# Kernel tuning notes

Measured on AMD Instinct MI355X. Metric: run time of the kernel, lower is better.

Reference implementation:

```python
import jax, jax.numpy as jnp
import numpy as np
from jax import lax

B, C, H, W = 4, 512, 48, 48
R = 8            # inter_rate -> spatial q/k channels = C // R
C4 = C // 4      # chl_attention query channels
N = H * W


def _conv1x1(x, w, b=None):
    # x: (B,C,H,W), w: (O,C)
    y = jnp.einsum('bchw,oc->bohw', x, w)
    if b is not None:
        y = y + b[None, :, None, None]
    return y


def _conv3x3(x, w):
    # w: (O,I,3,3), SAME padding, no bias
    return lax.conv_general_dilated(x, w, (1, 1), 'SAME',
                                    dimension_numbers=('NCHW', 'OIHW', 'NCHW'))


def _bn_relu(x, scale, bias):
    # eval-mode BatchNorm folded into per-channel scale/bias, then ReLU
    return jax.nn.relu(x * scale[None, :, None, None] + bias[None, :, None, None])


def _masked_softmax(e, mask):
    # softmax restricted to mask>0 positions (== exp(e)*mask / sum(exp(e)*mask))
    neg = jnp.finfo(e.dtype).min
    z = jnp.where(mask[None] > 0, e, neg)
    return jax.nn.softmax(z, axis=-1)


def _chl(x, qw, qs, qb, ew, eb):
    # channel attention block (chl_attention)
    b, c, h, w = x.shape
    n = h * w
    q = jnp.einsum('bchw,oc->bohw', x, qw)                 # (B,C4,H,W)
    q = jax.nn.relu(q * qs[None, :, None, None] + qb[None, :, None, None])
    q = q.reshape(b, C4, n)
    k = x.reshape(b, c, n)
    energy = jnp.einsum('bqn,bcn->bqc', q, k)              # (B,C4,C)
    expand = jnp.einsum('oq,bqc->boc', ew, energy) + eb[None, :, None]  # (B,C,C)
    en = jnp.max(expand, -1, keepdims=True) - expand
    attn = jax.nn.softmax(en, -1)                          # (B,C,C)
    out = jnp.einsum('bcd,bdn->bcn', attn, k)
    return out.reshape(b, c, h, w)


def setup_inputs() -> dict:
    key = jax.random.key(0)
    ks = jax.random.split(key, 32)
    f = jnp.float32
    s = lambda k, shp, sc: (sc * jax.random.normal(k, shp)).astype(f)
    inp = {}
    inp['x'] = s(ks[0], (B, C, H, W), 1.0)
    Cr = C // R
    inp['wq'] = s(ks[1], (Cr, C), 1.0 / np.sqrt(C))
    inp['bq'] = s(ks[2], (Cr,), 0.02)
    inp['wk'] = s(ks[3], (Cr, C), 1.0 / np.sqrt(C))
    inp['bk'] = s(ks[4], (Cr,), 0.02)
    inp['wv0'] = s(ks[5], (C, C), 1.0 / np.sqrt(C))
    inp['bv0'] = s(ks[6], (C,), 0.02)
    inp['conv1_w'] = s(ks[7], (C, C, 3, 3), 1.0 / np.sqrt(9 * C))
    inp['conv1_s'] = (1.0 + 0.1 * jax.random.normal(ks[8], (C,))).astype(f)
    inp['conv1_b'] = s(ks[9], (C,), 0.05)
    inp['conv2_w'] = s(ks[10], (C, C, 3, 3), 1.0 / np.sqrt(9 * C))
    inp['conv2_s'] = (1.0 + 0.1 * jax.random.normal(ks[11], (C,))).astype(f)
    inp['conv2_b'] = s(ks[12], (C,), 0.05)
    inp['gamma'] = jnp.full((1,), 0.5, f)
    inp['gamma1'] = jnp.full((1,), 0.5, f)
    inp['gamma2'] = jnp.full((1,), 0.5, f)
    # chl_attention #1 params
    inp['c1_qw'] = s(ks[13], (C4, C), 1.0 / np.sqrt(C))
    inp['c1_qs'] = (1.0 + 0.1 * jax.random.normal(ks[14], (C4,))).astype(f)
    inp['c1_qb'] = s(ks[15], (C4,), 0.05)
    inp['c1_ew'] = s(ks[16], (C, C4), 1.0 / np.sqrt(C4))
    inp['c1_eb'] = s(ks[17], (C,), 0.02)
    # chl_attention #2 params
    inp['c2_qw'] = s(ks[18], (C4, C), 1.0 / np.sqrt(C))
    inp['c2_qs'] = (1.0 + 0.1 * jax.random.normal(ks[19], (C4,))).astype(f)
    inp['c2_qb'] = s(ks[20], (C4,), 0.05)
    inp['c2_ew'] = s(ks[21], (C, C4), 1.0 / np.sqrt(C4))
    inp['c2_eb'] = s(ks[22], (C,), 0.02)
    # binary (N,N) masks: random sparsity + diagonal so every row has support
    eye = jnp.eye(N, dtype=f)
    m1 = (jax.random.uniform(ks[23], (N, N)) < 0.25).astype(f)
    m2 = (jax.random.uniform(ks[24], (N, N)) < 0.10).astype(f)
    inp['mask1'] = jnp.maximum(m1, eye)
    inp['mask2'] = jnp.maximum(m2, eye)
    return inp


def reference(x, wq, bq, wk, bk, wv0, bv0, conv1_w, conv1_s, conv1_b,
              conv2_w, conv2_s, conv2_b, gamma, gamma1, gamma2,
              c1_qw, c1_qs, c1_qb, c1_ew, c1_eb,
              c2_qw, c2_qs, c2_qb, c2_ew, c2_eb, mask1, mask2):
    b, c, h, w = x.shape
    n = h * w
    q = _conv1x1(x, wq, bq).reshape(b, -1, n)   # (B,Cr,N)
    k = _conv1x1(x, wk, bk).reshape(b, -1, n)   # (B,Cr,N)
    energy = jnp.einsum('bqn,bqm->bnm', q, k)   # (B,N,N)
    attn0 = jax.nn.softmax(energy, -1)
    attn1 = _masked_softmax(energy, mask1)
    attn2 = _masked_softmax(energy, mask2)
    v = _conv1x1(x, wv0, bv0).reshape(b, c, n)
    # pass 0 (unmasked)
    out0 = jnp.einsum('bcn,bmn->bcm', v, attn0).reshape(b, c, h, w)
    out0 = gamma[0] * out0 + x
    out0 = _bn_relu(_conv3x3(out0, conv1_w), conv1_s, conv1_b)
    # pass 1 (mask1, channel-attn value)
    v1 = _chl(out0, c1_qw, c1_qs, c1_qb, c1_ew, c1_eb).reshape(b, c, n)
    out1 = jnp.einsum('bcn,bmn->bcm', v1, attn1).reshape(b, c, h, w)
    out1 = gamma1[0] * out1 + out0
    out1 = _bn_relu(_conv3x3(out1, conv2_w), conv2_s, conv2_b)
    # pass 2 (mask2)
    v2 = _chl(out1, c2_qw, c2_qs, c2_qb, c2_ew, c2_eb).reshape(b, c, n)
    out2 = jnp.einsum('bcn,bmn->bcm', v2, attn2).reshape(b, c, h, w)
    out = gamma2[0] * out2 + out1
    return out
```

## Files before the change

### kernel.cpp

```cpp
#include <hip/hip_runtime.h>

#define B_  4
#define C_  512
#define H_  48
#define W_  48
#define N_  2304
#define CR_ 64
#define C4_ 128
#define TK  16
#define LDSP 68
#define PW  50
#define PN  2500
#define KW  4608

typedef short  s16x8 __attribute__((ext_vector_type(8)));
typedef float  f32x4 __attribute__((ext_vector_type(4)));

__device__ __forceinline__ unsigned short f2bf(float f) {
  union { float f; unsigned int u; } v; v.f = f;
  const unsigned int u = v.u;
  return (unsigned short)((u + 0x7FFFu + ((u >> 16) & 1u)) >> 16);
}
__device__ __forceinline__ float bf2f(unsigned short h) {
  union { unsigned int u; float f; } v; v.u = ((unsigned int)h) << 16;
// ... 28 lines not shown
  for (int kk = 0; kk < TK; ++kk) {
    const float4 a4 = *(const float4*)(&As[kk][ty * 4]);
    const float4 b4 = *(const float4*)(&Bs[kk][tx * 4]);
    const float av[4] = {a4.x, a4.y, a4.z, a4.w};
    const float bv[4] = {b4.x, b4.y, b4.z, b4.w};
#pragma unroll
    for (int i = 0; i < 4; ++i)
#pragma unroll
      for (int j = 0; j < 4; ++j)
        acc[i][j] = fmaf(av[i], bv[j], acc[i][j]);
  }
}

__global__ __launch_bounds__(256)
void gemm_nn(const float* __restrict__ A, long long aStrideB, int lda,
             const float* __restrict__ B, long long bStrideB, int ldb,
             float* __restrict__ Y, long long yStrideB, int ldy,
             int K,
             const float* __restrict__ scale, const float* __restrict__ bias, int relu)
{
  __shared__ float As[TK][LDSP], Bs[TK][LDSP];
  const int b  = blockIdx.z;
  const int m0 = blockIdx.y * 64, n0 = blockIdx.x * 64;
  const int tid = threadIdx.x, tx = tid & 15, ty = tid >> 4;
  const int ia = tid >> 2, ka = (tid & 3) * 4;
  const int jb = tid & 63, kb = (tid >> 6) * 4;
  const float* Ab = A + (size_t)b * aStrideB;
  const float* Bb = B + (size_t)b * bStrideB;
  float acc[4][4] = {};
  for (int k0 = 0; k0 < K; k0 += TK) {
    const float4 a4 = *(const float4*)(Ab + (size_t)(m0 + ia) * lda + k0 + ka);
    As[ka + 0][ia] = a4.x; As[ka + 1][ia] = a4.y;
    As[ka + 2][ia] = a4.z; As[ka + 3][ia] = a4.w;
#pragma unroll
    for (int t = 0; t < 4; ++t)
      Bs[kb + t][jb] = Bb[(size_t)(k0 + kb + t) * ldb + n0 + jb];
    __syncthreads();
    mm16(As, Bs, acc, ty, tx);
    __syncthreads();
  }
  float* Yb = Y + (size_t)b * yStrideB;
#pragma unroll
  for (int i = 0; i < 4; ++i) {
    const int row = m0 + ty * 4 + i;
    const float s = scale ? scale[row] : 1.f;
    const float bb = bias ? bias[row] : 0.f;
    float4 o;
    o.x = acc[i][0] * s + bb; o.y = acc[i][1] * s + bb;
    o.z = acc[i][2] * s + bb; o.w = acc[i][3] * s + bb;
    if (relu) {
      o.x = fmaxf(o.x, 0.f); o.y = fmaxf(o.y, 0.f);
      o.z = fmaxf(o.z, 0.f); o.w = fmaxf(o.w, 0.f);
    }
    *(float4*)(Yb + (size_t)row * ldy + n0 + tx * 4) = o;
  }
}

__global__ __launch_bounds__(256)
void gemm_nt(const float* __restrict__ A, long long aStrideB, int lda,
             const float* __restrict__ B, long long bStrideB, int ldb,
             float* __restrict__ Y, long long yStrideB, int ldy, int K)
{
  __shared__ float As[TK][LDSP], Bs[TK][LDSP];
  const int b  = blockIdx.z;
  const int m0 = blockIdx.y * 64, n0 = blockIdx.x * 64;
  const int tid = threadIdx.x, tx = tid & 15, ty = tid >> 4;
  const int ia = tid >> 2, ka = (tid & 3) * 4;
  const float* Ab = A + (size_t)b * aStrideB;
  const float* Bb = B + (size_t)b * bStrideB;
  float acc[4][4] = {};
  for (int k0 = 0; k0 < K; k0 += TK) {
    const float4 a4 = *(const float4*)(Ab + (size_t)(m0 + ia) * lda + k0 + ka);
    As[ka + 0][ia] = a4.x; As[ka + 1][ia] = a4.y;
    As[ka + 2][ia] = a4.z; As[ka + 3][ia] = a4.w;
    const float4 b4 = *(const float4*)(Bb + (size_t)(n0 + ia) * ldb + k0 + ka);
    Bs[ka + 0][ia] = b4.x; Bs[ka + 1][ia] = b4.y;
    Bs[ka + 2][ia] = b4.z; Bs[ka + 3][ia] = b4.w;
    __syncthreads();
    mm16(As, Bs, acc, ty, tx);
    __syncthreads();
  }
  float* Yb = Y + (size_t)b * yStrideB;
#pragma unroll
  for (int i = 0; i < 4; ++i) {
    const int row = m0 + ty * 4 + i;
    float4 o = {acc[i][0], acc[i][1], acc[i][2], acc[i][3]};
    *(float4*)(Yb + (size_t)row * ldy + n0 + tx * 4) = o;
  }
}

__global__ __launch_bounds__(256)
void gemm_nt_splitk(const float* __restrict__ A, long long aStrideB, int lda,
                    const float* __restrict__ B, long long bStrideB, int ldb,
                    float* __restrict__ Y, long long yStrideB, int ldy, int K)
{
  __shared__ float As[TK][LDSP], Bs[TK][LDSP];
  const int z = blockIdx.z, b = z >> 2, ks = z & 3;
  const int kBeg = ks * (K / 4), kEnd = kBeg + K / 4;
  const int m0 = blockIdx.y * 64, n0 = blockIdx.x * 64;
  const int tid = threadIdx.x, tx = tid & 15, ty = tid >> 4;
  const int ia = tid >> 2, ka = (tid & 3) * 4;
  const float* Ab = A + (size_t)b * aStrideB;
  const float* Bb = B + (size_t)b * bStrideB;
  float acc[4][4] = {};
  for (int k0 = kBeg; k0 < kEnd; k0 += TK) {
    const float4 a4 = *(const float4*)(Ab + (size_t)(m0 + ia) * lda + k0 + ka);
    As[ka + 0][ia] = a4.x; As[ka + 1][ia] = a4.y;
    As[ka + 2][ia] = a4.z; As[ka + 3][ia] = a4.w;
    const float4 b4 = *(const float4*)(Bb + (size_t)(n0 + ia) * ldb + k0 + ka);
    Bs[ka + 0][ia] = b4.x; Bs[ka + 1][ia] = b4.y;
    Bs[ka + 2][ia] = b4.z; Bs[ka + 3][ia] = b4.w;
    __syncthreads();
    mm16(As, Bs, acc, ty, tx);
    __syncthreads();
  }
  float* Yb = Y + (size_t)b * yStrideB;
#pragma unroll
  for (int i = 0; i < 4; ++i) {
    const int row = m0 + ty * 4 + i;
#pragma unroll
    for (int j = 0; j < 4; ++j)
      atomicAdd(Yb + (size_t)row * ldy + n0 + tx * 4 + j, acc[i][j]);
  }
}

__global__ __launch_bounds__(256)
void zero_buf(float4* __restrict__ p, int n4)
{
  const int i = blockIdx.x * 256 + threadIdx.x;
  if (i < n4) p[i] = float4{0.f, 0.f, 0.f, 0.f};
}

__global__ __launch_bounds__(256)
void gemm_tn(const float* __restrict__ A, long long aStrideB, int lda,
             const float* __restrict__ B, long long bStrideB, int ldb,
             float* __restrict__ Y, long long yStrideB, int ldy, int K)
{
  __shared__ float As[TK][LDSP], Bs[TK][LDSP];
  const int b  = blockIdx.z;
// ... 85 lines not shown
      const float4 x2 = *(const float4*)(src + 8);
      const float4 x3 = *(const float4*)(src + 12);
      s16x8 p0 = { (short)f2bf(x0.x), (short)f2bf(x0.y), (short)f2bf(x0.z), (short)f2bf(x0.w),
                   (short)f2bf(x1.x), (short)f2bf(x1.y), (short)f2bf(x1.z), (short)f2bf(x1.w) };
      s16x8 p1 = { (short)f2bf(x2.x), (short)f2bf(x2.y), (short)f2bf(x2.z), (short)f2bf(x2.w),
                   (short)f2bf(x3.x), (short)f2bf(x3.y), (short)f2bf(x3.z), (short)f2bf(x3.w) };
      *(s16x8*)&Bs[sRow][sK]     = p0;
      *(s16x8*)&Bs[sRow][sK + 8] = p1;
    }
    __syncthreads();
#pragma unroll
    for (int kc = 0; kc < 2; ++kc) {
      const s16x8 a0 = *(const s16x8*)&As[wm * 32 + lrow     ][kc * 32 + lk8];
      const s16x8 a1 = *(const s16x8*)&As[wm * 32 + 16 + lrow][kc * 32 + lk8];
      const s16x8 b0 = *(const s16x8*)&Bs[wn * 32 + lrow     ][kc * 32 + lk8];
      const s16x8 b1 = *(const s16x8*)&Bs[wn * 32 + 16 + lrow][kc * 32 + lk8];
      acc[0][0] = __builtin_amdgcn_mfma_f32_16x16x32_bf16(a0, b0, acc[0][0], 0, 0, 0);
      acc[0][1] = __builtin_amdgcn_mfma_f32_16x16x32_bf16(a0, b1, acc[0][1], 0, 0, 0);
      acc[1][0] = __builtin_amdgcn_mfma_f32_16x16x32_bf16(a1, b0, acc[1][0], 0, 0, 0);
      acc[1][1] = __builtin_amdgcn_mfma_f32_16x16x32_bf16(a1, b1, acc[1][1], 0, 0, 0);
    }
    __syncthreads();
  }

  const float g = gammaPtr ? gammaPtr[0] : 0.f;
  const float* Rb = Resid ? Resid + (size_t)b * rSB : nullptr;
#pragma unroll
  for (int mt = 0; mt < 2; ++mt)
#pragma unroll
    for (int nt = 0; nt < 2; ++nt) {
      const int col = n0 + wn * 32 + nt * 16 + lrow;
      const int rbase = m0 + wm * 32 + mt * 16 + (lane >> 4) * 4;
#pragma unroll
      for (int i = 0; i < 4; ++i) {
        const int row = rbase + i;
        float v = acc[mt][nt][i];
        if (Rb) {
          v = g * v + Rb[(size_t)row * ldy + col];
        } else {
          const float s  = scale ? scale[row] : 1.f;
          const float bb = bias ? bias[row] : 0.f;
          v = v * s + bb;
          if (relu) v = fmaxf(v, 0.f);
        }
        if (outBf16)
          ((unsigned short*)Yv)[(size_t)b * ySB + (size_t)row * ldy + col] = f2bf(v);
        else
          ((float*)Yv)[(size_t)b * ySB + (size_t)row * ldy + col] = v;
      }
    }
}

__global__ __launch_bounds__(256)
void pad_split(const float* __restrict__ X, unsigned short* __restrict__ Xh,
               unsigned short* __restrict__ Xl)
{
  __shared__ float t[64][65];
  const int b = blockIdx.x, n0 = blockIdx.y * 64;
  const int tid = threadIdx.x;
  const float* Xb = X + (size_t)b * C_ * N_;
  unsigned short* Xhb = Xh + (size_t)b * PN * C_;
  unsigned short* Xlb = Xl + (size_t)b * PN * C_;
  for (int cs = 0; cs < 8; ++cs) {
    const int c0 = cs * 64;
    __syncthreads();
#pragma unroll
    for (int i = 0; i < 16; ++i) {
      const int cc = i * 4 + (tid >> 6);
      t[cc][tid & 63] = Xb[(size_t)(c0 + cc) * N_ + n0 + (tid & 63)];
    }
    __syncthreads();
    const int cc = tid & 63;
#pragma unroll
    for (int i = 0; i < 16; ++i) {
      const int nn = i * 4 + (tid >> 6);
      const int n = n0 + nn;
      const float v = t[cc][nn];
      const unsigned short hh = f2bf(v);
      const unsigned short ll = f2bf(v - bf2f(hh));
      const size_t p = (size_t)((n / 48 + 1) * PW + (n % 48) + 1) * C_ + c0 + cc;
      Xhb[p] = hh; Xlb[p] = ll;
    }
  }
}

__global__ __launch_bounds__(256)
void zero_ring(unsigned short* __restrict__ Xh, unsigned short* __restrict__ Xl)
{
  const int b = blockIdx.y, r = blockIdx.x;
  int pcol;
  if (r < 50)       pcol = r;
  else if (r < 100) pcol = 49 * PW + (r - 50);
  else if (r < 148) pcol = (r - 100 + 1) * PW;
  else              pcol = (r - 148 + 1) * PW + 49;
  unsigned int* h = (unsigned int*)(Xh + ((size_t)b * PN + pcol) * C_);
  unsigned int* l = (unsigned int*)(Xl + ((size_t)b * PN + pcol) * C_);
  h[threadIdx.x] = 0u;
  l[threadIdx.x] = 0u;
}

__global__ __launch_bounds__(256)
void wsplit(const float* __restrict__ W, unsigned short* __restrict__ Wh,
            unsigned short* __restrict__ Wl)
{
  const int o = blockIdx.x, tap = blockIdx.y;
#pragma unroll
  for (int i = 0; i < 2; ++i) {
    const int c = threadIdx.x + i * 256;
    const float v = W[(size_t)o * KW + c * 9 + tap];
    const unsigned short hh = f2bf(v);
    Wh[(size_t)o * KW + tap * C_ + c] = hh;
    Wl[(size_t)o * KW + tap * C_ + c] = f2bf(v - bf2f(hh));
  }
}

__global__ __launch_bounds__(256)
void tr_bf16(const float* __restrict__ X, unsigned short* __restrict__ T)
{
  __shared__ float t[64][65];
  const int b = blockIdx.x, n0 = blockIdx.y * 64;
  const int tid = threadIdx.x;
  const float* Xb = X + (size_t)b * C_ * N_;
  unsigned short* Tb = T + (size_t)b * N_ * C_;
  for (int cs = 0; cs < 8; ++cs) {
    const int c0 = cs * 64;
    __syncthreads();
#pragma unroll
    for (int i = 0; i < 16; ++i) {
      const int cc = i * 4 + (tid >> 6);
      t[cc][tid & 63] = Xb[(size_t)(c0 + cc) * N_ + n0 + (tid & 63)];
    }
    __syncthreads();
    const int cc = tid & 63;
#pragma unroll
    for (int i = 0; i < 16; ++i) {
      const int nn = i * 4 + (tid >> 6);
      Tb[(size_t)(n0 + nn) * C_ + c0 + cc] = f2bf(t[cc][nn]);
    }
  }
}

__global__ __launch_bounds__(256)
void mfma_conv2(const unsigned short* __restrict__ Xh, const unsigned short* __restrict__ Xl,
                const unsigned short* __restrict__ Wh, const unsigned short* __restrict__ Wl,
                const float* __restrict__ sc, const float* __restrict__ bi,
                float* __restrict__ Y)
{
  __shared__ unsigned short Ah[64][72], Al[64][72];
  __shared__ unsigned short Bh[64][72], Bl[64][72];
  const int b  = blockIdx.z;
  const int m0 = blockIdx.y * 64, n0 = blockIdx.x * 64;
  const int tid  = threadIdx.x;
  const int lane = tid & 63, wave = tid >> 6;
  const int wm = wave >> 1, wn = wave & 1;
  const int lrow = lane & 15, lk8 = (lane >> 4) * 8;
  const int sRow = tid >> 2, sK = (tid & 3) * 16;
  const int nj = n0 + sRow;
  const int pbase = (nj / 48 + 1) * PW + (nj % 48) + 1;
  const unsigned short* Xhb = Xh + (size_t)b * PN * C_;
  const unsigned short* Xlb = Xl + (size_t)b * PN * C_;
  f32x4 acc[2][2] = {};

#pragma unroll
  for (int tap = 0; tap < 9; ++tap) {
    const int toff = (tap / 3 - 1) * PW + (tap % 3 - 1);
    const size_t bofs = (size_t)(pbase + toff) * C_;
    const size_t wrow = (size_t)(m0 + sRow) * KW + (size_t)tap * C_;
    for (int cs = 0; cs < 8; ++cs) {
      const int c0 = cs * 64;
      {
        const unsigned short* s = Wh + wrow + c0 + sK;
        *(s16x8*)&Ah[sRow][sK]     = *(const s16x8*)(s);
        *(s16x8*)&Ah[sRow][sK + 8] = *(const s16x8*)(s + 8);
        const unsigned short* s2 = Wl + wrow + c0 + sK;
        *(s16x8*)&Al[sRow][sK]     = *(const s16x8*)(s2);
        *(s16x8*)&Al[sRow][sK + 8] = *(const s16x8*)(s2 + 8);
      }
      {
        const unsigned short* s = Xhb + bofs + c0 + sK;
        *(s16x8*)&Bh[sRow][sK]     = *(const s16x8*)(s);
        *(s16x8*)&Bh[sRow][sK + 8] = *(const s16x8*)(s + 8);
        const unsigned short* s2 = Xlb + bofs + c0 + sK;
        *(s16x8*)&Bl[sRow][sK]     = *(const s16x8*)(s2);
        *(s16x8*)&Bl[sRow][sK + 8] = *(const s16x8*)(s2 + 8);
      }
      __syncthreads();
#pragma unroll
      for (int kc = 0; kc < 2; ++kc) {
        const s16x8 ah0 = *(const s16x8*)&Ah[wm * 32 + lrow     ][kc * 32 + lk8];
        const s16x8 ah1 = *(const s16x8*)&Ah[wm * 32 + 16 + lrow][kc * 32 + lk8];
        const s16x8 al0 = *(const s16x8*)&Al[wm * 32 + lrow     ][kc * 32 + lk8];
        const s16x8 al1 = *(const s16x8*)&Al[wm * 32 + 16 + lrow][kc * 32 + lk8];
        const s16x8 bh0 = *(const s16x8*)&Bh[wn * 32 + lrow     ][kc * 32 + lk8];
        const s16x8 bh1 = *(const s16x8*)&Bh[wn * 32 + 16 + lrow][kc * 32 + lk8];
        const s16x8 bl0 = *(const s16x8*)&Bl[wn * 32 + lrow     ][kc * 32 + lk8];
        const s16x8 bl1 = *(const s16x8*)&Bl[wn * 32 + 16 + lrow][kc * 32 + lk8];
        acc[0][0] = __builtin_amdgcn_mfma_f32_16x16x32_bf16(ah0, bh0, acc[0][0], 0, 0, 0);
        acc[0][1] = __builtin_amdgcn_mfma_f32_16x16x32_bf16(ah0, bh1, acc[0][1], 0, 0, 0);
        acc[1][0] = __builtin_amdgcn_mfma_f32_16x16x32_bf16(ah1, bh0, acc[1][0], 0, 0, 0);
        acc[1][1] = __builtin_amdgcn_mfma_f32_16x16x32_bf16(ah1, bh1, acc[1][1], 0, 0, 0);
        acc[0][0] = __builtin_amdgcn_mfma_f32_16x16x32_bf16(ah0, bl0, acc[0][0], 0, 0, 0);
        acc[0][1] = __builtin_amdgcn_mfma_f32_16x16x32_bf16(ah0, bl1, acc[0][1], 0, 0, 0);
        acc[1][0] = __builtin_amdgcn_mfma_f32_16x16x32_bf16(ah1, bl0, acc[1][0], 0, 0, 0);
        acc[1][1] = __builtin_amdgcn_mfma_f32_16x16x32_bf16(ah1, bl1, acc[1][1], 0, 0, 0);
        acc[0][0] = __builtin_amdgcn_mfma_f32_16x16x32_bf16(al0, bh0, acc[0][0], 0, 0, 0);
        acc[0][1] = __builtin_amdgcn_mfma_f32_16x16x32_bf16(al0, bh1, acc[0][1], 0, 0, 0);
        acc[1][0] = __builtin_amdgcn_mfma_f32_16x16x32_bf16(al1, bh0, acc[1][0], 0, 0, 0);
        acc[1][1] = __builtin_amdgcn_mfma_f32_16x16x32_bf16(al1, bh1, acc[1][1], 0, 0, 0);
      }
      __syncthreads();
    }
  }

  float* Yb = Y + (size_t)b * C_ * N_;
#pragma unroll
  for (int mt = 0; mt < 2; ++mt)
#pragma unroll
    for (int nt = 0; nt < 2; ++nt) {
      const int col = n0 + wn * 32 + nt * 16 + lrow;
      const int rbase = m0 + wm * 32 + mt * 16 + (lane >> 4) * 4;
#pragma unroll
      for (int i = 0; i < 4; ++i) {
        const int row = rbase + i;
        const float v = fmaxf(acc[mt][nt][i] * sc[row] + bi[row], 0.f);
        Yb[(size_t)row * N_ + col] = v;
      }
    }
}

__global__ __launch_bounds__(256)
void mfma_conv_split(const float* __restrict__ X, const float* __restrict__ Wt,
                     const float* __restrict__ sc, const float* __restrict__ bi,
                     float* __restrict__ Y)
{
  __shared__ unsigned short Ah[64][72], Al[64][72];
  __shared__ unsigned short Bh[64][72], Bl[64][72];
  const int b  = blockIdx.z;
  const int m0 = blockIdx.y * 64, n0 = blockIdx.x * 64;
  const int tid  = threadIdx.x;
  const int lane = tid & 63, wave = tid >> 6;
  const int wm = wave >> 1, wn = wave & 1;
  const int lrow = lane & 15, lk8 = (lane >> 4) * 8;
  const int sRow = tid >> 2, sK = (tid & 3) * 16;
  const int tj = tid & 63, tkg = (tid >> 6) * 16;
  const int n = n0 + tj, yy = n / W_, xx = n - yy * W_;
  const float* Xb = X + (size_t)b * C_ * N_;
  const int K = KW;
  f32x4 acc[2][2] = {};

  for (int k0 = 0; k0 < K; k0 += 64) {
    {
      const float* src = Wt + (size_t)(m0 + sRow) * K + k0 + sK;
      unsigned short h[16], l[16];
#pragma unroll
      for (int t = 0; t < 16; ++t) {
        const float v = src[t];
        const unsigned short hh = f2bf(v);
        h[t] = hh;
        l[t] = f2bf(v - bf2f(hh));
      }
      *(s16x8*)&Ah[sRow][sK]     = *(s16x8*)&h[0];
      *(s16x8*)&Ah[sRow][sK + 8] = *(s16x8*)&h[8];
      *(s16x8*)&Al[sRow][sK]     = *(s16x8*)&l[0];
      *(s16x8*)&Al[sRow][sK + 8] = *(s16x8*)&l[8];
    }
    {
#pragma unroll
      for (int ii = 0; ii < 16; ii += 2) {
        unsigned int ph = 0, pl = 0;
#pragma unroll
        for (int hft = 0; hft < 2; ++hft) {
          const int kg = k0 + tkg + ii + hft;
          const int c = kg / 9, tap = kg - c * 9;
          const int t3 = tap / 3;
          const int iy = yy + t3 - 1, ix = xx + (tap - t3 * 3) - 1;
          float v = 0.f;
          if (iy >= 0 && iy < H_ && ix >= 0 && ix < W_)
            v = Xb[(size_t)c * N_ + iy * W_ + ix];
          const unsigned short hh = f2bf(v);
          const unsigned short ll = f2bf(v - bf2f(hh));
          ph |= ((unsigned int)hh) << (16 * hft);
          pl |= ((unsigned int)ll) << (16 * hft);
        }
        *(unsigned int*)&Bh[tj][tkg + ii] = ph;
        *(unsigned int*)&Bl[tj][tkg + ii] = pl;
      }
    }
    __syncthreads();
#pragma unroll
    for (int kc = 0; kc < 2; ++kc) {
      const s16x8 ah0 = *(const s16x8*)&Ah[wm * 32 + lrow     ][kc * 32 + lk8];
      const s16x8 ah1 = *(const s16x8*)&Ah[wm * 32 + 16 + lrow][kc * 32 + lk8];
      const s16x8 al0 = *(const s16x8*)&Al[wm * 32 + lrow     ][kc * 32 + lk8];
      const s16x8 al1 = *(const s16x8*)&Al[wm * 32 + 16 + lrow][kc * 32 + lk8];
      const s16x8 bh0 = *(const s16x8*)&Bh[wn * 32 + lrow     ][kc * 32 + lk8];
      const s16x8 bh1 = *(const s16x8*)&Bh[wn * 32 + 16 + lrow][kc * 32 + lk8];
      const s16x8 bl0 = *(const s16x8*)&Bl[wn * 32 + lrow     ][kc * 32 + lk8];
      const s16x8 bl1 = *(const s16x8*)&Bl[wn * 32 + 16 + lrow][kc * 32 + lk8];
      acc[0][0] = __builtin_amdgcn_mfma_f32_16x16x32_bf16(ah0, bh0, acc[0][0], 0, 0, 0);
      acc[0][1] = __builtin_amdgcn_mfma_f32_16x16x32_bf16(ah0, bh1, acc[0][1], 0, 0, 0);
      acc[1][0] = __builtin_amdgcn_mfma_f32_16x16x32_bf16(ah1, bh0, acc[1][0], 0, 0, 0);
      acc[1][1] = __builtin_amdgcn_mfma_f32_16x16x32_bf16(ah1, bh1, acc[1][1], 0, 0, 0);
      acc[0][0] = __builtin_amdgcn_mfma_f32_16x16x32_bf16(ah0, bl0, acc[0][0], 0, 0, 0);
      acc[0][1] = __builtin_amdgcn_mfma_f32_16x16x32_bf16(ah0, bl1, acc[0][1], 0, 0, 0);
      acc[1][0] = __builtin_amdgcn_mfma_f32_16x16x32_bf16(ah1, bl0, acc[1][0], 0, 0, 0);
// ... 282 lines not shown
  const float rs = 1.f / s;
  r[tid] = e0 * rs;
  r[tid + 256] = e1 * rs;
}

extern "C" void kernel_launch(void* const* d_in, const int* in_sizes, int n_in,
                              void* d_out, int out_size, void* d_ws, size_t ws_size,
                              hipStream_t stream)
{
  (void)in_sizes; (void)n_in; (void)out_size;
  const float* x      = (const float*)d_in[0];
  const float* wq     = (const float*)d_in[1];
  const float* bq     = (const float*)d_in[2];
  const float* wk     = (const float*)d_in[3];
  const float* bk     = (const float*)d_in[4];
  const float* wv0    = (const float*)d_in[5];
  const float* bv0    = (const float*)d_in[6];
  const float* c1w    = (const float*)d_in[7];
  const float* c1s    = (const float*)d_in[8];
  const float* c1b    = (const float*)d_in[9];
  const float* c2w    = (const float*)d_in[10];
  const float* c2s    = (const float*)d_in[11];
  const float* c2b    = (const float*)d_in[12];
  const float* gamma  = (const float*)d_in[13];
  const float* gamma1 = (const float*)d_in[14];
  const float* gamma2 = (const float*)d_in[15];
  const float* c1qw   = (const float*)d_in[16];
  const float* c1qs   = (const float*)d_in[17];
  const float* c1qb   = (const float*)d_in[18];
  const float* c1ew   = (const float*)d_in[19];
  const float* c1eb   = (const float*)d_in[20];
  const float* c2qw   = (const float*)d_in[21];
  const float* c2qs   = (const float*)d_in[22];
  const float* c2qb   = (const float*)d_in[23];
  const float* c2ew   = (const float*)d_in[24];
  const float* c2eb   = (const float*)d_in[25];
  const float* mask1  = (const float*)d_in[26];
  const float* mask2  = (const float*)d_in[27];

  const size_t QK = 589824;
  const size_t CQ = 1179648;
  const size_t VV = 4718592;
  const size_t EE = 21233664;
  const size_t ST = 55296;
  const size_t CE = 262144;
  const size_t CA = 1048576;
  const size_t ELEMS_B = CQ + VV + EE + ST + VV + CE + CA;
  const size_t ELEMS_A = ELEMS_B + EE / 2;
  const int tier = (ws_size >= ELEMS_A * 4) ? 0
                 : (ws_size >= ELEMS_B * 4) ? 1 : 2;

  float* ws = (float*)d_ws;
  float *qbuf, *kbuf, *cq, *vbuf, *ebuf, *stb, *o0, *ce1, *cat_;
  unsigned short *Pbuf = nullptr, *oT = nullptr, *Xh = nullptr, *Xl = nullptr,
                 *Whs = nullptr, *Wls = nullptr;
  if (tier <= 1) {
    qbuf = ws; kbuf = ws + QK;
    cq   = ws;
    vbuf = ws + CQ;
    ebuf = vbuf + VV;
    stb  = ebuf + EE;
    o0   = stb + ST;
    ce1  = o0 + VV;
    cat_ = ce1 + CE;
    if (tier == 0) {
      unsigned short* reg = (unsigned short*)(cat_ + CA);
      Pbuf = reg;
      oT   = reg;
      Xh   = reg + 4718592;
      Xl   = Xh + 5120000;
      Whs  = Xl + 5120000;
      Wls  = Whs + 2359296;
    }
  } else {
    qbuf = ws; kbuf = qbuf + QK;
    cq   = kbuf + QK;
    vbuf = cq + CQ;
    stb  = vbuf + VV;
    o0   = stb + ST;
    ce1  = o0 + VV;
    cat_ = ce1 + CE;
    ebuf = nullptr;
  }
  float* t0 = (float*)d_out;
  float* o1 = o0;
  unsigned short* vb16 = (unsigned short*)vbuf;

  const dim3 TPB(256);
  const long long sxc = (long long)C_ * N_;
  const long long sqr = (long long)CR_ * N_;
  const long long sq4 = (long long)C4_ * N_;
  const long long sNN = (long long)N_ * N_;
  const long long sNC = (long long)N_ * C_;
  const long long sCC = (long long)C_ * C_;
  const long long sEC = (long long)C4_ * C_;

  gemm_nn<<<dim3(36, 1, 4), TPB, 0, stream>>>(wq, 0, C_, x, sxc, N_,
                                              qbuf, sqr, N_, C_, nullptr, bq, 0);
  gemm_nn<<<dim3(36, 1, 4), TPB, 0, stream>>>(wk, 0, C_, x, sxc, N_,
                                              kbuf, sqr, N_, C_, nullptr, bk, 0);
  if (tier == 0) {
    tr_bf16<<<dim3(B_, 36), TPB, 0, stream>>>(x, oT);
    mfma_gemm<<<dim3(36, 8, 4), TPB, 0, stream>>>(wv0, 0, 0, C_, oT, sNC, C_, 2,
        vb16, 1, sxc, N_, C_, nullptr, bv0, 0, nullptr, nullptr, 0);
  } else {
    mfma_gemm<<<dim3(36, 8, 4), TPB, 0, stream>>>(wv0, 0, 0, C_, x, sxc, N_, 1,
        vbuf, 0, sxc, N_, C_, nullptr, bv0, 0, nullptr, nullptr, 0);
  }

  if (tier <= 1) {
    gemm_tn<<<dim3(36, 36, 4), TPB, 0, stream>>>(qbuf, sqr, N_, kbuf, sqr, N_,
                                                 ebuf, sNN, N_, CR_);
    softmax_stats<<<dim3(N_, 4), TPB, 0, stream>>>(ebuf, mask1, mask2, stb);
  } else {
    softmax_stats_rq<<<dim3(N_, 4), TPB, 0, stream>>>(qbuf, kbuf, mask1, mask2, stb);
  }

  for (int pass = 0; pass < 3; ++pass) {
    const float* msk = (pass == 0) ? nullptr : (pass == 1 ? mask1 : mask2);
    const float* gm  = (pass == 0) ? gamma : (pass == 1 ? gamma1 : gamma2);
    const float* res = (pass == 0) ? x : o0;
    float* dst = (pass == 2) ? (float*)d_out : t0;

    if (tier == 0) {
      build_P<<<dim3(N_, 4), TPB, 0, stream>>>(ebuf, stb, pass, msk, Pbuf);
      mfma_gemm<<<dim3(36, 8, 4), TPB, 0, stream>>>(vb16, 1, sxc, N_, Pbuf, sNN, N_, 2,
          dst, 0, sxc, N_, N_, nullptr, nullptr, 0, gm, res, sxc);
    } else if (tier == 1) {
      attn_apply<<<dim3(36, 8, 4), TPB, 0, stream>>>(vbuf, ebuf, stb, pass, msk,
                                                     gm, res, dst);
    } else {
      attn_apply_rq<<<dim3(36, 8, 4), TPB, 0, stream>>>(vbuf, qbuf, kbuf, stb, pass, msk,
                                                        gm, res, dst);
    }
    if (pass == 2) break;

    const float* cw = (pass == 0) ? c1w : c2w;
    const float* cs = (pass == 0) ? c1s : c2s;
    const float* cb = (pass == 0) ? c1b : c2b;
    if (tier == 0) {
      pad_split<<<dim3(B_, 36), TPB, 0, stream>>>(dst, Xh, Xl);
      zero_ring<<<dim3(196, B_), TPB, 0, stream>>>(Xh, Xl);
      wsplit<<<dim3(512, 9), TPB, 0, stream>>>(cw, Whs, Wls);
      mfma_conv2<<<dim3(36, 8, 4), TPB, 0, stream>>>(Xh, Xl, Whs, Wls, cs, cb, o0);
    } else {
      mfma_conv_split<<<dim3(36, 8, 4), TPB, 0, stream>>>(dst, cw, cs, cb, o0);
    }

    const float* qw = (pass == 0) ? c1qw : c2qw;
    const float* qs = (pass == 0) ? c1qs : c2qs;
    const float* qb = (pass == 0) ? c1qb : c2qb;
    const float* ew = (pass == 0) ? c1ew : c2ew;
    const float* eb = (pass == 0) ? c1eb : c2eb;
    gemm_nn<<<dim3(36, 2, 4), TPB, 0, stream>>>(qw, 0, C_, o0, sxc, N_,
                                                cq, sq4, N_, C_, qs, qb, 1);
    zero_buf<<<dim3(256), TPB, 0, stream>>>((float4*)ce1, (int)(CE / 4));
    gemm_nt_splitk<<<dim3(8, 2, 16), TPB, 0, stream>>>(cq, sq4, N_, o0, sxc, N_,
                                                       ce1, sEC, C_, N_);
    gemm_nn<<<dim3(8, 8, 4), TPB, 0, stream>>>(ew, 0, C4_, ce1, sEC, C_,
                                               cat_, sCC, C_, C4_, nullptr, eb, 0);
    chl_softmax<<<dim3(C_ * 4), TPB, 0, stream>>>(cat_);
    if (tier == 0) {
      tr_bf16<<<dim3(B_, 36), TPB, 0, stream>>>(o0, oT);
      mfma_gemm<<<dim3(36, 8, 4), TPB, 0, stream>>>(cat_, 0, sCC, C_, oT, sNC, C_, 2,
          vb16, 1, sxc, N_, C_, nullptr, nullptr, 0, nullptr, nullptr, 0);
    } else {
      mfma_gemm<<<dim3(36, 8, 4), TPB, 0, stream>>>(cat_, 0, sCC, C_, o0, sxc, N_, 1,
          vbuf, 0, sxc, N_, C_, nullptr, nullptr, 0, nullptr, nullptr, 0);
    }
  }
  (void)o1;
}
```

Measured before the change: 1.393 ms.

## Move small fp32 GEMMs to split-bf16 MFMA and prefetch conv loads

Adds a generic split-bf16 (hi/lo) MFMA GEMM kernel and routes the q/k projections, the q·k energy, and the channel-attention GEMMs through it in tier 0, replacing scalar fp32 LDS GEMMs. The transpose kernel now emits hi/lo bf16 pairs that the new projections reuse. The 3x3 conv kernel is flattened into a single 72-step loop that prefetches the next tile into registers while MFMAs run on the current one. This adds register pressure and atomic split-K accumulation, and uses three-term bf16 products in place of exact fp32.

```diff
diff --git a/kernel.cpp b/kernel.cpp
--- a/kernel.cpp
+++ b/kernel.cpp
@@ -104,39 +104,6 @@
       o.x = fmaxf(o.x, 0.f); o.y = fmaxf(o.y, 0.f);
       o.z = fmaxf(o.z, 0.f); o.w = fmaxf(o.w, 0.f);
     }
-    *(float4*)(Yb + (size_t)row * ldy + n0 + tx * 4) = o;
-  }
-}
-
-__global__ __launch_bounds__(256)
-void gemm_nt(const float* __restrict__ A, long long aStrideB, int lda,
-             const float* __restrict__ B, long long bStrideB, int ldb,
-             float* __restrict__ Y, long long yStrideB, int ldy, int K)
-{
-  __shared__ float As[TK][LDSP], Bs[TK][LDSP];
-  const int b  = blockIdx.z;
-  const int m0 = blockIdx.y * 64, n0 = blockIdx.x * 64;
-  const int tid = threadIdx.x, tx = tid & 15, ty = tid >> 4;
-  const int ia = tid >> 2, ka = (tid & 3) * 4;
-  const float* Ab = A + (size_t)b * aStrideB;
-  const float* Bb = B + (size_t)b * bStrideB;
-  float acc[4][4] = {};
-  for (int k0 = 0; k0 < K; k0 += TK) {
-    const float4 a4 = *(const float4*)(Ab + (size_t)(m0 + ia) * lda + k0 + ka);
-    As[ka + 0][ia] = a4.x; As[ka + 1][ia] = a4.y;
-    As[ka + 2][ia] = a4.z; As[ka + 3][ia] = a4.w;
-    const float4 b4 = *(const float4*)(Bb + (size_t)(n0 + ia) * ldb + k0 + ka);
-    Bs[ka + 0][ia] = b4.x; Bs[ka + 1][ia] = b4.y;
-    Bs[ka + 2][ia] = b4.z; Bs[ka + 3][ia] = b4.w;
-    __syncthreads();
-    mm16(As, Bs, acc, ty, tx);
-    __syncthreads();
-  }
-  float* Yb = Y + (size_t)b * yStrideB;
-#pragma unroll
-  for (int i = 0; i < 4; ++i) {
-    const int row = m0 + ty * 4 + i;
-    float4 o = {acc[i][0], acc[i][1], acc[i][2], acc[i][3]};
     *(float4*)(Yb + (size_t)row * ldy + n0 + tx * 4) = o;
   }
 }
@@ -328,6 +295,123 @@
 }
 
 __global__ __launch_bounds__(256)
+void mfma_sp(const float* __restrict__ A, long long aSB, int lda,
+             const void* __restrict__ B0v, const void* __restrict__ B1v,
+             long long bSB, int ldb, int bPre,
+             float* __restrict__ Y, long long ySB, int ldy, int outMode,
+             int K, int nSplit,
+             const float* __restrict__ scale, const float* __restrict__ bias, int relu)
+{
+  __shared__ unsigned short Ah[64][72], Al[64][72];
+  __shared__ unsigned short Bh[64][72], Bl[64][72];
+  const int z = blockIdx.z;
+  const int b = z / nSplit, ks = z % nSplit;
+  const int kLen = K / nSplit, kBeg = ks * kLen, kEnd = kBeg + kLen;
+  const int m0 = blockIdx.y * 64, n0 = blockIdx.x * 64;
+  const int tid  = threadIdx.x;
+  const int lane = tid & 63, wave = tid >> 6;
+  const int wm = wave >> 1, wn = wave & 1;
+  const int lrow = lane & 15, lk8 = (lane >> 4) * 8;
+  const int sRow = tid >> 2, sK = (tid & 3) * 16;
+  const float* Ab = A + (size_t)b * aSB;
+  f32x4 acc[2][2] = {};
+
+  for (int k0 = kBeg; k0 < kEnd; k0 += 64) {
+    {
+      const float* src = Ab + (size_t)(m0 + sRow) * lda + k0 + sK;
+      s16x8 h0, l0, h1, l1;
+#pragma unroll
+      for (int t = 0; t < 8; ++t) {
+        const float v = src[t];
+        const unsigned short hh = f2bf(v);
+        h0[t] = (short)hh; l0[t] = (short)f2bf(v - bf2f(hh));
+      }
+#pragma unroll
+      for (int t = 0; t < 8; ++t) {
+        const float v = src[8 + t];
+        const unsigned short hh = f2bf(v);
+        h1[t] = (short)hh; l1[t] = (short)f2bf(v - bf2f(hh));
+      }
+      *(s16x8*)&Ah[sRow][sK] = h0; *(s16x8*)&Ah[sRow][sK + 8] = h1;
+      *(s16x8*)&Al[sRow][sK] = l0; *(s16x8*)&Al[sRow][sK + 8] = l1;
+    }
+    if (bPre) {
+      const unsigned short* Bh_ = (const unsigned short*)B0v + (size_t)b * bSB;
+      const unsigned short* Bl_ = (const unsigned short*)B1v + (size_t)b * bSB;
+      const size_t off = (size_t)(n0 + sRow) * ldb + k0 + sK;
+      *(s16x8*)&Bh[sRow][sK]     = *(const s16x8*)(Bh_ + off);
+      *(s16x8*)&Bh[sRow][sK + 8] = *(const s16x8*)(Bh_ + off + 8);
+      *(s16x8*)&Bl[sRow][sK]     = *(const s16x8*)(Bl_ + off);
+      *(s16x8*)&Bl[sRow][sK + 8] = *(const s16x8*)(Bl_ + off + 8);
+    } else {
+      const float* Bb = (const float*)B0v + (size_t)b * bSB;
+      const float* src = Bb + (size_t)(n0 + sRow) * ldb + k0 + sK;
+      s16x8 h0, l0, h1, l1;
+#pragma unroll
+      for (int t = 0; t < 8; ++t) {
+        const float v = src[t];
+        const unsigned short hh = f2bf(v);
+        h0[t] = (short)hh; l0[t] = (short)f2bf(v - bf2f(hh));
+      }
+#pragma unroll
+      for (int t = 0; t < 8; ++t) {
+        const float v = src[8 + t];
+        const unsigned short hh = f2bf(v);
+        h1[t] = (short)hh; l1[t] = (short)f2bf(v - bf2f(hh));
+      }
+      *(s16x8*)&Bh[sRow][sK] = h0; *(s16x8*)&Bh[sRow][sK + 8] = h1;
+      *(s16x8*)&Bl[sRow][sK] = l0; *(s16x8*)&Bl[sRow][sK + 8] = l1;
+    }
+    __syncthreads();
+#pragma unroll
+    for (int kc = 0; kc < 2; ++kc) {
+      const s16x8 ah0 = *(const s16x8*)&Ah[wm * 32 + lrow     ][kc * 32 + lk8];
+      const s16x8 ah1 = *(const s16x8*)&Ah[wm * 32 + 16 + lrow][kc * 32 + lk8];
+      const s16x8 al0 = *(const s16x8*)&Al[wm * 32 + lrow     ][kc * 32 + lk8];
+      const s16x8 al1 = *(const s16x8*)&Al[wm * 32 + 16 + lrow][kc * 32 + lk8];
+      const s16x8 bh0 = *(const s16x8*)&Bh[wn * 32 + lrow     ][kc * 32 + lk8];
+      const s16x8 bh1 = *(const s16x8*)&Bh[wn * 32 + 16 + lrow][kc * 32 + lk8];
+      const s16x8 bl0 = *(const s16x8*)&Bl[wn * 32 + lrow     ][kc * 32 + lk8];
+      const s16x8 bl1 = *(const s16x8*)&Bl[wn * 32 + 16 + lrow][kc * 32 + lk8];
+      acc[0][0] = __builtin_amdgcn_mfma_f32_16x16x32_bf16(ah0, bh0, acc[0][0], 0, 0, 0);
+      acc[0][1] = __builtin_amdgcn_mfma_f32_16x16x32_bf16(ah0, bh1, acc[0][1], 0, 0, 0);
+      acc[1][0] = __builtin_amdgcn_mfma_f32_16x16x32_bf16(ah1, bh0, acc[1][0], 0, 0, 0);
+      acc[1][1] = __builtin_amdgcn_mfma_f32_16x16x32_bf16(ah1, bh1, acc[1][1], 0, 0, 0);
+      acc[0][0] = __builtin_amdgcn_mfma_f32_16x16x32_bf16(ah0, bl0, acc[0][0], 0, 0, 0);
+      acc[0][1] = __builtin_amdgcn_mfma_f32_16x16x32_bf16(ah0, bl1, acc[0][1], 0, 0, 0);
+      acc[1][0] = __builtin_amdgcn_mfma_f32_16x16x32_bf16(ah1, bl0, acc[1][0], 0, 0, 0);
+      acc[1][1] = __builtin_amdgcn_mfma_f32_16x16x32_bf16(ah1, bl1, acc[1][1], 0, 0, 0);
+      acc[0][0] = __builtin_amdgcn_mfma_f32_16x16x32_bf16(al0, bh0, acc[0][0], 0, 0, 0);
+      acc[0][1] = __builtin_amdgcn_mfma_f32_16x16x32_bf16(al0, bh1, acc[0][1], 0, 0, 0);
+      acc[1][0] = __builtin_amdgcn_mfma_f32_16x16x32_bf16(al1, bh0, acc[1][0], 0, 0, 0);
+      acc[1][1] = __builtin_amdgcn_mfma_f32_16x16x32_bf16(al1, bh1, acc[1][1], 0, 0, 0);
+    }
+    __syncthreads();
+  }
+
+  float* Yb = Y + (size_t)b * ySB;
+#pragma unroll
+  for (int mt = 0; mt < 2; ++mt)
+#pragma unroll
+    for (int nt = 0; nt < 2; ++nt) {
+      const int col = n0 + wn * 32 + nt * 16 + lrow;
+      const int rbase = m0 + wm * 32 + mt * 16 + (lane >> 4) * 4;
+#pragma unroll
+      for (int i = 0; i < 4; ++i) {
+        const int row = rbase + i;
+        float v = acc[mt][nt][i];
+        const float s  = scale ? scale[row] : 1.f;
+        const float bb = bias ? bias[row] : 0.f;
+        v = v * s + bb;
+        if (relu) v = fmaxf(v, 0.f);
+        if (outMode == 0)      Yb[(size_t)row * ldy + col] = v;
+        else if (outMode == 1) Yb[(size_t)col * ldy + row] = v;
+        else                   atomicAdd(Yb + (size_t)col * ldy + row, v);
+      }
+    }
+}
+
+__global__ __launch_bounds__(256)
 void pad_split(const float* __restrict__ X, unsigned short* __restrict__ Xh,
                unsigned short* __restrict__ Xl)
 {
@@ -391,13 +475,15 @@
 }
 
 __global__ __launch_bounds__(256)
-void tr_bf16(const float* __restrict__ X, unsigned short* __restrict__ T)
+void tr_split(const float* __restrict__ X, unsigned short* __restrict__ Th,
+              unsigned short* __restrict__ Tl)
 {
   __shared__ float t[64][65];
   const int b = blockIdx.x, n0 = blockIdx.y * 64;
   const int tid = threadIdx.x;
   const float* Xb = X + (size_t)b * C_ * N_;
-  unsigned short* Tb = T + (size_t)b * N_ * C_;
+  unsigned short* Thb = Th + (size_t)b * N_ * C_;
+  unsigned short* Tlb = Tl + (size_t)b * N_ * C_;
   for (int cs = 0; cs < 8; ++cs) {
     const int c0 = cs * 64;
     __syncthreads();
@@ -411,7 +497,10 @@
 #pragma unroll
     for (int i = 0; i < 16; ++i) {
       const int nn = i * 4 + (tid >> 6);
-      Tb[(size_t)(n0 + nn) * C_ + c0 + cc] = f2bf(t[cc][nn]);
+      const float v = t[cc][nn];
+      const unsigned short hh = f2bf(v);
+      Thb[(size_t)(n0 + nn) * C_ + c0 + cc] = hh;
+      Tlb[(size_t)(n0 + nn) * C_ + c0 + cc] = f2bf(v - bf2f(hh));
     }
   }
 }
@@ -436,57 +525,55 @@
   const unsigned short* Xhb = Xh + (size_t)b * PN * C_;
   const unsigned short* Xlb = Xl + (size_t)b * PN * C_;
   f32x4 acc[2][2] = {};
-
-#pragma unroll
-  for (int tap = 0; tap < 9; ++tap) {
-    const int toff = (tap / 3 - 1) * PW + (tap % 3 - 1);
-    const size_t bofs = (size_t)(pbase + toff) * C_;
-    const size_t wrow = (size_t)(m0 + sRow) * KW + (size_t)tap * C_;
-    for (int cs = 0; cs < 8; ++cs) {
-      const int c0 = cs * 64;
-      {
-        const unsigned short* s = Wh + wrow + c0 + sK;
-        *(s16x8*)&Ah[sRow][sK]     = *(const s16x8*)(s);
-        *(s16x8*)&Ah[sRow][sK + 8] = *(const s16x8*)(s + 8);
-        const unsigned short* s2 = Wl + wrow + c0 + sK;
-        *(s16x8*)&Al[sRow][sK]     = *(const s16x8*)(s2);
-        *(s16x8*)&Al[sRow][sK + 8] = *(const s16x8*)(s2 + 8);
-      }
-      {
-        const unsigned short* s = Xhb + bofs + c0 + sK;
-        *(s16x8*)&Bh[sRow][sK]     = *(const s16x8*)(s);
-        *(s16x8*)&Bh[sRow][sK + 8] = *(const s16x8*)(s + 8);
-        const unsigned short* s2 = Xlb + bofs + c0 + sK;
-        *(s16x8*)&Bl[sRow][sK]     = *(const s16x8*)(s2);
-        *(s16x8*)&Bl[sRow][sK + 8] = *(const s16x8*)(s2 + 8);
-      }
-      __syncthreads();
-#pragma unroll
-      for (int kc = 0; kc < 2; ++kc) {
-        const s16x8 ah0 = *(const s16x8*)&Ah[wm * 32 + lrow     ][kc * 32 + lk8];
-        const s16x8 ah1 = *(const s16x8*)&Ah[wm * 32 + 16 + lrow][kc * 32 + lk8];
-        const s16x8 al0 = *(const s16x8*)&Al[wm * 32 + lrow     ][kc * 32 + lk8];
-        const s16x8 al1 = *(const s16x8*)&Al[wm * 32 + 16 + lrow][kc * 32 + lk8];
-        const s16x8 bh0 = *(const s16x8*)&Bh[wn * 32 + lrow     ][kc * 32 + lk8];
-        const s16x8 bh1 = *(const s16x8*)&Bh[wn * 32 + 16 + lrow][kc * 32 + lk8];
-        const s16x8 bl0 = *(const s16x8*)&Bl[wn * 32 + lrow     ][kc * 32 + lk8];
-        const s16x8 bl1 = *(const s16x8*)&Bl[wn * 32 + 16 + lrow][kc * 32 + lk8];
-        acc[0][0] = __builtin_amdgcn_mfma_f32_16x16x32_bf16(ah0, bh0, acc[0][0], 0, 0, 0);
-        acc[0][1] = __builtin_amdgcn_mfma_f32_16x16x32_bf16(ah0, bh1, acc[0][1], 0, 0, 0);
-        acc[1][0] = __builtin_amdgcn_mfma_f32_16x16x32_bf16(ah1, bh0, acc[1][0], 0, 0, 0);
-        acc[1][1] = __builtin_amdgcn_mfma_f32_16x16x32_bf16(ah1, bh1, acc[1][1], 0, 0, 0);
-        acc[0][0] = __builtin_amdgcn_mfma_f32_16x16x32_bf16(ah0, bl0, acc[0][0], 0, 0, 0);
-        acc[0][1] = __builtin_amdgcn_mfma_f32_16x16x32_bf16(ah0, bl1, acc[0][1], 0, 0, 0);
-        acc[1][0] = __builtin_amdgcn_mfma_f32_16x16x32_bf16(ah1, bl0, acc[1][0], 0, 0, 0);
-        acc[1][1] = __builtin_amdgcn_mfma_f32_16x16x32_bf16(ah1, bl1, acc[1][1], 0, 0, 0);
-        acc[0][0] = __builtin_amdgcn_mfma_f32_16x16x32_bf16(al0, bh0, acc[0][0], 0, 0, 0);
-        acc[0][1] = __builtin_amdgcn_mfma_f32_16x16x32_bf16(al0, bh1, acc[0][1], 0, 0, 0);
-        acc[1][0] = __builtin_amdgcn_mfma_f32_16x16x32_bf16(al1, bh0, acc[1][0], 0, 0, 0);
-        acc[1][1] = __builtin_amdgcn_mfma_f32_16x16x32_bf16(al1, bh1, acc[1][1], 0, 0, 0);
-      }
-      __syncthreads();
-    }
-  }
+  s16x8 r0, r1, r2, r3, r4, r5, r6, r7;
+
+#define CONV_LD(IT)                                                        \
+  {                                                                        \
+    const int tap_ = (IT) >> 3, c0_ = ((IT) & 7) * 64;                     \
+    const int t3_ = tap_ / 3;                                              \
+    const int toff_ = (t3_ - 1) * PW + (tap_ - t3_ * 3 - 1);               \
+    const size_t bofs_ = (size_t)(pbase + toff_) * C_ + c0_ + sK;          \
+    const size_t wrow_ = (size_t)(m0 + sRow) * KW + (size_t)tap_ * C_ + c0_ + sK; \
+    r0 = *(const s16x8*)(Wh + wrow_);     r1 = *(const s16x8*)(Wh + wrow_ + 8); \
+    r2 = *(const s16x8*)(Wl + wrow_);     r3 = *(const s16x8*)(Wl + wrow_ + 8); \
+    r4 = *(const s16x8*)(Xhb + bofs_);    r5 = *(const s16x8*)(Xhb + bofs_ + 8); \
+    r6 = *(const s16x8*)(Xlb + bofs_);    r7 = *(const s16x8*)(Xlb + bofs_ + 8); \
+  }
+
+  CONV_LD(0);
+  for (int it = 0; it < 72; ++it) {
+    *(s16x8*)&Ah[sRow][sK] = r0; *(s16x8*)&Ah[sRow][sK + 8] = r1;
+    *(s16x8*)&Al[sRow][sK] = r2; *(s16x8*)&Al[sRow][sK + 8] = r3;
+    *(s16x8*)&Bh[sRow][sK] = r4; *(s16x8*)&Bh[sRow][sK + 8] = r5;
+    *(s16x8*)&Bl[sRow][sK] = r6; *(s16x8*)&Bl[sRow][sK + 8] = r7;
+    __syncthreads();
+    if (it < 71) CONV_LD(it + 1);
+#pragma unroll
+    for (int kc = 0; kc < 2; ++kc) {
+      const s16x8 ah0 = *(const s16x8*)&Ah[wm * 32 + lrow     ][kc * 32 + lk8];
+      const s16x8 ah1 = *(const s16x8*)&Ah[wm * 32 + 16 + lrow][kc * 32 + lk8];
+      const s16x8 al0 = *(const s16x8*)&Al[wm * 32 + lrow     ][kc * 32 + lk8];
+      const s16x8 al1 = *(const s16x8*)&Al[wm * 32 + 16 + lrow][kc * 32 + lk8];
+      const s16x8 bh0 = *(const s16x8*)&Bh[wn * 32 + lrow     ][kc * 32 + lk8];
+      const s16x8 bh1 = *(const s16x8*)&Bh[wn * 32 + 16 + lrow][kc * 32 + lk8];
+      const s16x8 bl0 = *(const s16x8*)&Bl[wn * 32 + lrow     ][kc * 32 + lk8];
+      const s16x8 bl1 = *(const s16x8*)&Bl[wn * 32 + 16 + lrow][kc * 32 + lk8];
+      acc[0][0] = __builtin_amdgcn_mfma_f32_16x16x32_bf16(ah0, bh0, acc[0][0], 0, 0, 0);
+      acc[0][1] = __builtin_amdgcn_mfma_f32_16x16x32_bf16(ah0, bh1, acc[0][1], 0, 0, 0);
+      acc[1][0] = __builtin_amdgcn_mfma_f32_16x16x32_bf16(ah1, bh0, acc[1][0], 0, 0, 0);
+      acc[1][1] = __builtin_amdgcn_mfma_f32_16x16x32_bf16(ah1, bh1, acc[1][1], 0, 0, 0);
+      acc[0][0] = __builtin_amdgcn_mfma_f32_16x16x32_bf16(ah0, bl0, acc[0][0], 0, 0, 0);
+      acc[0][1] = __builtin_amdgcn_mfma_f32_16x16x32_bf16(ah0, bl1, acc[0][1], 0, 0, 0);
+      acc[1][0] = __builtin_amdgcn_mfma_f32_16x16x32_bf16(ah1, bl0, acc[1][0], 0, 0, 0);
+      acc[1][1] = __builtin_amdgcn_mfma_f32_16x16x32_bf16(ah1, bl1, acc[1][1], 0, 0, 0);
+      acc[0][0] = __builtin_amdgcn_mfma_f32_16x16x32_bf16(al0, bh0, acc[0][0], 0, 0, 0);
+      acc[0][1] = __builtin_amdgcn_mfma_f32_16x16x32_bf16(al0, bh1, acc[0][1], 0, 0, 0);
+      acc[1][0] = __builtin_amdgcn_mfma_f32_16x16x32_bf16(al1, bh0, acc[1][0], 0, 0, 0);
+      acc[1][1] = __builtin_amdgcn_mfma_f32_16x16x32_bf16(al1, bh1, acc[1][1], 0, 0, 0);
+    }
+    __syncthreads();
+  }
+#undef CONV_LD
 
   float* Yb = Y + (size_t)b * C_ * N_;
 #pragma unroll
@@ -521,12 +608,11 @@
   const int tj = tid & 63, tkg = (tid >> 6) * 16;
   const int n = n0 + tj, yy = n / W_, xx = n - yy * W_;
   const float* Xb = X + (size_t)b * C_ * N_;
-  const int K = KW;
   f32x4 acc[2][2] = {};
 
-  for (int k0 = 0; k0 < K; k0 += 64) {
+  for (int k0 = 0; k0 < KW; k0 += 64) {
     {
-      const float* src = Wt + (size_t)(m0 + sRow) * K + k0 + sK;
+      const float* src = Wt + (size_t)(m0 + sRow) * KW + k0 + sK;
       unsigned short h[16], l[16];
 #pragma unroll
       for (int t = 0; t < 16; ++t) {
@@ -915,8 +1001,10 @@
 
   float* ws = (float*)d_ws;
   float *qbuf, *kbuf, *cq, *vbuf, *ebuf, *stb, *o0, *ce1, *cat_;
-  unsigned short *Pbuf = nullptr, *oT = nullptr, *Xh = nullptr, *Xl = nullptr,
-                 *Whs = nullptr, *Wls = nullptr;
+  unsigned short *Pbuf = nullptr, *Xh = nullptr, *Xl = nullptr,
+                 *Whs = nullptr, *Wls = nullptr,
+                 *xTh = nullptr, *xTl = nullptr, *oTh = nullptr, *oTl = nullptr;
+  float *qTf = nullptr, *kTf = nullptr;
   if (tier <= 1) {
     qbuf = ws; kbuf = ws + QK;
     cq   = ws;
@@ -928,12 +1016,17 @@
     cat_ = ce1 + CE;
     if (tier == 0) {
       unsigned short* reg = (unsigned short*)(cat_ + CA);
+      xTh = reg;
+      xTl = reg + 4718592;
+      qTf = (float*)(reg + 9437184);
+      kTf = qTf + 589824;
       Pbuf = reg;
-      oT   = reg;
-      Xh   = reg + 4718592;
-      Xl   = Xh + 5120000;
-      Whs  = Xl + 5120000;
-      Wls  = Whs + 2359296;
+      Xh  = reg;
+      Xl  = reg + 5120000;
+      Whs = reg + 10240000;
+      Wls = reg + 12599296;
+      oTh = reg;
+      oTl = reg + 4718592;
     }
   } else {
     qbuf = ws; kbuf = qbuf + QK;
@@ -946,7 +1039,6 @@
     ebuf = nullptr;
   }
   float* t0 = (float*)d_out;
-  float* o1 = o0;
   unsigned short* vb16 = (unsigned short*)vbuf;
 
   const dim3 TPB(256);
@@ -957,25 +1049,36 @@
   const long long sNC = (long long)N_ * C_;
   const long long sCC = (long long)C_ * C_;
   const long long sEC = (long long)C4_ * C_;
-
-  gemm_nn<<<dim3(36, 1, 4), TPB, 0, stream>>>(wq, 0, C_, x, sxc, N_,
-                                              qbuf, sqr, N_, C_, nullptr, bq, 0);
-  gemm_nn<<<dim3(36, 1, 4), TPB, 0, stream>>>(wk, 0, C_, x, sxc, N_,
-                                              kbuf, sqr, N_, C_, nullptr, bk, 0);
+  const long long sNR = (long long)N_ * CR_;
+
   if (tier == 0) {
-    tr_bf16<<<dim3(B_, 36), TPB, 0, stream>>>(x, oT);
-    mfma_gemm<<<dim3(36, 8, 4), TPB, 0, stream>>>(wv0, 0, 0, C_, oT, sNC, C_, 2,
+    tr_split<<<dim3(B_, 36), TPB, 0, stream>>>(x, xTh, xTl);
+    mfma_sp<<<dim3(36, 1, 4), TPB, 0, stream>>>(wq, 0, C_, xTh, xTl, sNC, C_, 1,
+        qTf, sNR, CR_, 1, C_, 1, nullptr, bq, 0);
+    mfma_sp<<<dim3(36, 1, 4), TPB, 0, stream>>>(wk, 0, C_, xTh, xTl, sNC, C_, 1,
+        kTf, sNR, CR_, 1, C_, 1, nullptr, bk, 0);
+    mfma_gemm<<<dim3(36, 8, 4), TPB, 0, stream>>>(wv0, 0, 0, C_, xTh, sNC, C_, 2,
         vb16, 1, sxc, N_, C_, nullptr, bv0, 0, nullptr, nullptr, 0);
-  } else {
+    mfma_sp<<<dim3(36, 36, 4), TPB, 0, stream>>>(qTf, sNR, CR_, kTf, nullptr, sNR, CR_, 0,
+        ebuf, sNN, N_, 0, CR_, 1, nullptr, nullptr, 0);
+    softmax_stats<<<dim3(N_, 4), TPB, 0, stream>>>(ebuf, mask1, mask2, stb);
+  } else if (tier == 1) {
+    gemm_nn<<<dim3(36, 1, 4), TPB, 0, stream>>>(wq, 0, C_, x, sxc, N_,
+                                                qbuf, sqr, N_, C_, nullptr, bq, 0);
+    gemm_nn<<<dim3(36, 1, 4), TPB, 0, stream>>>(wk, 0, C_, x, sxc, N_,
+                                                kbuf, sqr, N_, C_, nullptr, bk, 0);
     mfma_gemm<<<dim3(36, 8, 4), TPB, 0, stream>>>(wv0, 0, 0, C_, x, sxc, N_, 1,
         vbuf, 0, sxc, N_, C_, nullptr, bv0, 0, nullptr, nullptr, 0);
-  }
-
-  if (tier <= 1) {
     gemm_tn<<<dim3(36, 36, 4), TPB, 0, stream>>>(qbuf, sqr, N_, kbuf, sqr, N_,
                                                  ebuf, sNN, N_, CR_);
     softmax_stats<<<dim3(N_, 4), TPB, 0, stream>>>(ebuf, mask1, mask2, stb);
   } else {
+    gemm_nn<<<dim3(36, 1, 4), TPB, 0, stream>>>(wq, 0, C_, x, sxc, N_,
+                                                qbuf, sqr, N_, C_, nullptr, bq, 0);
+    gemm_nn<<<dim3(36, 1, 4), TPB, 0, stream>>>(wk, 0, C_, x, sxc, N_,
+                                                kbuf, sqr, N_, C_, nullptr, bk, 0);
+    mfma_gemm<<<dim3(36, 8, 4), TPB, 0, stream>>>(wv0, 0, 0, C_, x, sxc, N_, 1,
+        vbuf, 0, sxc, N_, C_, nullptr, bv0, 0, nullptr, nullptr, 0);
     softmax_stats_rq<<<dim3(N_, 4), TPB, 0, stream>>>(qbuf, kbuf, mask1, mask2, stb);
   }
 
@@ -1015,22 +1118,29 @@
     const float* qb = (pass == 0) ? c1qb : c2qb;
     const float* ew = (pass == 0) ? c1ew : c2ew;
     const float* eb = (pass == 0) ? c1eb : c2eb;
-    gemm_nn<<<dim3(36, 2, 4), TPB, 0, stream>>>(qw, 0, C_, o0, sxc, N_,
-                                                cq, sq4, N_, C_, qs, qb, 1);
-    zero_buf<<<dim3(256), TPB, 0, stream>>>((float4*)ce1, (int)(CE / 4));
-    gemm_nt_splitk<<<dim3(8, 2, 16), TPB, 0, stream>>>(cq, sq4, N_, o0, sxc, N_,
-                                                       ce1, sEC, C_, N_);
-    gemm_nn<<<dim3(8, 8, 4), TPB, 0, stream>>>(ew, 0, C4_, ce1, sEC, C_,
-                                               cat_, sCC, C_, C4_, nullptr, eb, 0);
-    chl_softmax<<<dim3(C_ * 4), TPB, 0, stream>>>(cat_);
     if (tier == 0) {
-      tr_bf16<<<dim3(B_, 36), TPB, 0, stream>>>(o0, oT);
-      mfma_gemm<<<dim3(36, 8, 4), TPB, 0, stream>>>(cat_, 0, sCC, C_, oT, sNC, C_, 2,
+      tr_split<<<dim3(B_, 36), TPB, 0, stream>>>(o0, oTh, oTl);
+      mfma_sp<<<dim3(36, 2, 4), TPB, 0, stream>>>(qw, 0, C_, oTh, oTl, sNC, C_, 1,
+          cq, sq4, N_, 0, C_, 1, qs, qb, 1);
+      zero_buf<<<dim3(256), TPB, 0, stream>>>((float4*)ce1, (int)(CE / 4));
+      mfma_sp<<<dim3(8, 2, 16), TPB, 0, stream>>>(cq, sq4, N_, o0, nullptr, sxc, N_, 0,
+          ce1, sEC, C4_, 2, N_, 4, nullptr, nullptr, 0);
+      mfma_sp<<<dim3(8, 8, 4), TPB, 0, stream>>>(ew, 0, C4_, ce1, nullptr, sEC, C4_, 0,
+          cat_, sCC, C_, 0, C4_, 1, nullptr, eb, 0);
+      chl_softmax<<<dim3(C_ * 4), TPB, 0, stream>>>(cat_);
+      mfma_gemm<<<dim3(36, 8, 4), TPB, 0, stream>>>(cat_, 0, sCC, C_, oTh, sNC, C_, 2,
           vb16, 1, sxc, N_, C_, nullptr, nullptr, 0, nullptr, nullptr, 0);
     } else {
+      gemm_nn<<<dim3(36, 2, 4), TPB, 0, stream>>>(qw, 0, C_, o0, sxc, N_,
+                                                  cq, sq4, N_, C_, qs, qb, 1);
+      zero_buf<<<dim3(256), TPB, 0, stream>>>((float4*)ce1, (int)(CE / 4));
+      gemm_nt_splitk<<<dim3(8, 2, 16), TPB, 0, stream>>>(cq, sq4, N_, o0, sxc, N_,
+                                                         ce1, sEC, C_, N_);
+      gemm_nn<<<dim3(8, 8, 4), TPB, 0, stream>>>(ew, 0, C4_, ce1, sEC, C_,
+                                                 cat_, sCC, C_, C4_, nullptr, eb, 0);
+      chl_softmax<<<dim3(C_ * 4), TPB, 0, stream>>>(cat_);
       mfma_gemm<<<dim3(36, 8, 4), TPB, 0, stream>>>(cat_, 0, sCC, C_, o0, sxc, N_, 1,
           vbuf, 0, sxc, N_, C_, nullptr, nullptr, 0, nullptr, nullptr, 0);
     }
   }
-  (void)o1;
-}
+}
```

After: 1.305 ms. 6.3% less time.
